# Kernel optimization log

Hardware: AMD Instinct MI355X
Metric: run time of the kernel (lower is better)

## Reference

```python
import jax, jax.numpy as jnp
import numpy as np

# Production-scale 3D conv: B=4, C=64->64, 32^3 volume, 3x3x3 kernel, stride 1, pad 1.
B, CIN, COUT = 4, 64, 64
KSIZE = (3, 3, 3)
STRIDE = (1, 1, 1)
PAD = 1
SPATIAL = (32, 32, 32)


def setup_inputs() -> dict:
    key = jax.random.key(0)
    k1, k2, k3 = jax.random.split(key, 3)
    x = jax.random.normal(k1, (B, CIN) + SPATIAL, dtype=jnp.float32)
    weight = jax.random.normal(k2, (COUT, CIN) + KSIZE, dtype=jnp.float32)
    bias = jax.random.normal(k3, (COUT,), dtype=jnp.float32)
    return {"x": x, "weight": weight, "bias": bias}


def reference(x, weight, bias):
    # The original materializes all sliding-window patches via nested unfold and
    # contracts with einsum('bci...,oci->bo...'). That is exactly a standard
    # cross-correlation (torch-style conv). We express the same math as a direct
    # convolution, avoiding the O(kernel_volume) patch blowup.
    out = jax.lax.conv_general_dilated(
        x,
        weight,
        window_strides=STRIDE,
        padding=[(PAD, PAD)] * 3,
        dimension_numbers=("NCDHW", "OIDHW", "NCDHW"),
    )
    return out + bias.reshape(1, -1, 1, 1, 1)
```

## Files before the change

kernel.cpp:

```cpp
#include <hip/hip_runtime.h>
#include <hip/hip_bf16.h>

#define WS_W_OFF    0
#define WS_ZERO_OFF 221184
#define WS_XT_OFF   262144

typedef __attribute__((ext_vector_type(8))) short s16x8;
typedef __attribute__((ext_vector_type(4))) float f32x4;

#define GLOBAL_AS __attribute__((address_space(1)))
#define LDS_AS    __attribute__((address_space(3)))

__device__ __forceinline__ unsigned short f2bf(float f) {
  unsigned u = __builtin_bit_cast(unsigned, f);
  u = u + 0x7fffu + ((u >> 16) & 1u);
  return (unsigned short)(u >> 16);
}

__global__ void prep_kernel(const float* __restrict__ x,
                            const float* __restrict__ w,
                            unsigned short* __restrict__ wsw,
                            float* __restrict__ zeros,
                            unsigned short* __restrict__ xt) {
  int blk = blockIdx.x;
  if (blk < 432) {
    int t = blk * 256 + threadIdx.x;
    int tap  = t % 27;
    int cin  = (t / 27) & 63;
    int cout = t / (27 * 64);
    int h   = cin >> 5;
    int q   = (cin >> 3) & 3;
    int j   = cin & 7;
    int nf  = cout >> 4;
    int lane = q * 16 + (cout & 15);
    int dst = (((tap * 2 + h) * 4 + nf) * 64 + lane) * 8 + j;
    wsw[dst] = f2bf(w[t]);
    if (t < 64) zeros[t] = 0.0f;
  } else {
    int t  = (blk - 432) * 256 + threadIdx.x;
    int s  = t & 32767;
    int c8 = (t >> 15) & 7;
    int b  = t >> 18;
    const float* src = x + (size_t)(b * 64 + c8 * 8) * 32768 + s;
    s16x8 v;
    #pragma unroll
    for (int k = 0; k < 8; ++k) v[k] = (short)f2bf(src[(size_t)k * 32768]);
    *(s16x8*)(xt + (size_t)(b * 32768 + s) * 64 + c8 * 8) = v;
  }
}

__global__ __launch_bounds__(128, 2) void conv_kernel(const float* __restrict__ bias,
                                                      float* __restrict__ out,
                                                      const char* __restrict__ ws) {
  __shared__ unsigned char halo[39 * 1024];

  const int tid  = threadIdx.x;
  const int lane = tid & 63;
  const int w    = tid >> 6;
  const int logical = (blockIdx.x & 7) * 128 + (blockIdx.x >> 3);
  const int yt = logical & 7, z = (logical >> 3) & 31, b = logical >> 8;
  const int y0 = yt * 4;

  const int r15 = lane & 15;
  const int hi4 = lane >> 4;

  const int sl_sub   = lane >> 2;
  const int sl_chunk = lane & 3;

  auto stage = [&](int h) {
    for (int g = w; g < 39; g += 2) {
      int pos = g * 16 + sl_sub;
      int hz = pos / 204; int rem = pos - hz * 204;
      int hy = rem / 34;  int hx = rem - hy * 34;
      int gz = z + hz - 1, gy = y0 + hy - 1, gx = hx - 1;
      bool inb = (pos < 612) & ((unsigned)gz < 32u) &
                 ((unsigned)gy < 32u) & ((unsigned)gx < 32u);
      int s = (gz * 32 + gy) * 32 + gx;
      int src = inb ? (WS_XT_OFF + (b * 32768 + s) * 128 + h * 64 + sl_chunk * 16)
                    : WS_ZERO_OFF;
      __builtin_amdgcn_global_load_lds(
          (const GLOBAL_AS void*)(ws + src),
          (LDS_AS void*)(&halo[g * 1024 + lane * 16]),
          16, 0, 0);
    }
  };

  const s16x8* __restrict__ wfr = (const s16x8*)(ws + WS_W_OFF);

  f32x4 zero4 = {0.f, 0.f, 0.f, 0.f};
  f32x4 acc[4][4];
  #pragma unroll
  for (int mf = 0; mf < 4; ++mf)
    #pragma unroll
    for (int nf = 0; nf < 4; ++nf) acc[mf][nf] = zero4;

  s16x8 B0[4], B1[4], A0[4], A1[4];

  auto loadB = [&](s16x8* dst, int h, int tap) {
    #pragma unroll
    for (int nf = 0; nf < 4; ++nf)
      dst[nf] = wfr[((tap * 2 + h) * 4 + nf) * 64 + lane];
  };

  auto loadA = [&](s16x8* a, int tap) {
    int kd = tap / 9; int r9 = tap - kd * 9;
    int kh = r9 / 3;  int kw = r9 - kh * 3;
    int prow = (kd * 6 + 2 * w + kh) * 34 + kw + r15;
    #pragma unroll
    for (int mf = 0; mf < 4; ++mf) {
      int pos = prow + (mf >> 1) * 34 + (mf & 1) * 16;
      a[mf] = *(const s16x8*)&halo[pos * 64 + hi4 * 16];
    }
  };

  auto compute = [&](const s16x8* a, const s16x8* B) {
    #pragma unroll
    for (int mf = 0; mf < 4; ++mf)
      #pragma unroll
      for (int nf = 0; nf < 4; ++nf)
        acc[mf][nf] = __builtin_amdgcn_mfma_f32_16x16x32_bf16(
            a[mf], B[nf], acc[mf][nf], 0, 0, 0);
  };

  #pragma unroll 1
  for (int h = 0; h < 2; ++h) {
    if (h) __syncthreads();
    stage(h);
    loadB(B0, h, 0);
    __syncthreads();
    loadA(A0, 0);
    for (int t = 0; t < 13; ++t) {
      loadB(B1, h, 2 * t + 1); loadA(A1, 2 * t + 1); compute(A0, B0);
      loadB(B0, h, 2 * t + 2); loadA(A0, 2 * t + 2); compute(A1, B1);
    }
    compute(A0, B0);
  }

  #pragma unroll
  for (int nf = 0; nf < 4; ++nf) {
    int cout = nf * 16 + r15;
    float bv = bias[cout];
    #pragma unroll
    for (int mf = 0; mf < 4; ++mf) {
      int y  = y0 + 2 * w + (mf >> 1);
      int x0 = (mf & 1) * 16 + 4 * hi4;
      float* orow = out + ((size_t)((b * 64 + cout) * 32 + z) * 32 + y) * 32;
      f32x4 v;
      #pragma unroll
      for (int r = 0; r < 4; ++r) v[r] = acc[mf][nf][r] + bv;
      *(f32x4*)&orow[x0] = v;
    }
  }
}

extern "C" void kernel_launch(void* const* d_in, const int* in_sizes, int n_in,
                              void* d_out, int out_size, void* d_ws, size_t ws_size,
                              hipStream_t stream) {
  const float* x    = (const float*)d_in[0];
  const float* wgt  = (const float*)d_in[1];
  const float* bias = (const float*)d_in[2];
  float* out = (float*)d_out;
  char* ws = (char*)d_ws;

  prep_kernel<<<4528, 256, 0, stream>>>(x, wgt,
                                        (unsigned short*)(ws + WS_W_OFF),
                                        (float*)(ws + WS_ZERO_OFF),
                                        (unsigned short*)(ws + WS_XT_OFF));
  conv_kernel<<<1024, 128, 0, stream>>>(bias, out, ws);
}
```

Baseline: 49.07 us.

## Tile two z-slices per block with four waves and triple-buffer tap loads

Each block now computes a 2×4×32 output tile (two z planes) with four waves instead of one z plane with two waves. The staged halo grows from 3 to 4 z-planes, so the halo load per output point drops, since neighbouring z planes share two input planes. The tap loop becomes a three-stage rotating register buffer for A and B fragments, with B preloaded before the barrier. The cost is more LDS per block (52 KB), which may limit occupancy, more registers for the extra buffers, and only 512 blocks, which reduces parallelism across CUs.

```diff
diff --git a/kernel.cpp b/kernel.cpp
--- a/kernel.cpp
+++ b/kernel.cpp
@@ -49,17 +49,19 @@
   }
 }
 
-__global__ __launch_bounds__(128, 2) void conv_kernel(const float* __restrict__ bias,
+__global__ __launch_bounds__(256, 2) void conv_kernel(const float* __restrict__ bias,
                                                       float* __restrict__ out,
                                                       const char* __restrict__ ws) {
-  __shared__ unsigned char halo[39 * 1024];
+  __shared__ unsigned char halo[52 * 1024];
 
   const int tid  = threadIdx.x;
   const int lane = tid & 63;
   const int w    = tid >> 6;
-  const int logical = (blockIdx.x & 7) * 128 + (blockIdx.x >> 3);
-  const int yt = logical & 7, z = (logical >> 3) & 31, b = logical >> 8;
-  const int y0 = yt * 4;
+  const int logical = (blockIdx.x & 7) * 64 + (blockIdx.x >> 3);
+  const int yt = logical & 7, zt = (logical >> 3) & 15, b = logical >> 7;
+  const int z0 = zt * 2, y0 = yt * 4;
+  const int zo  = w >> 1;
+  const int yo2 = (w & 1) * 2;
 
   const int r15 = lane & 15;
   const int hi4 = lane >> 4;
@@ -68,12 +70,12 @@
   const int sl_chunk = lane & 3;
 
   auto stage = [&](int h) {
-    for (int g = w; g < 39; g += 2) {
+    for (int g = w; g < 52; g += 4) {
       int pos = g * 16 + sl_sub;
       int hz = pos / 204; int rem = pos - hz * 204;
       int hy = rem / 34;  int hx = rem - hy * 34;
-      int gz = z + hz - 1, gy = y0 + hy - 1, gx = hx - 1;
-      bool inb = (pos < 612) & ((unsigned)gz < 32u) &
+      int gz = z0 + hz - 1, gy = y0 + hy - 1, gx = hx - 1;
+      bool inb = (pos < 816) & ((unsigned)gz < 32u) &
                  ((unsigned)gy < 32u) & ((unsigned)gx < 32u);
       int s = (gz * 32 + gy) * 32 + gx;
       int src = inb ? (WS_XT_OFF + (b * 32768 + s) * 128 + h * 64 + sl_chunk * 16)
@@ -94,7 +96,7 @@
     #pragma unroll
     for (int nf = 0; nf < 4; ++nf) acc[mf][nf] = zero4;
 
-  s16x8 B0[4], B1[4], A0[4], A1[4];
+  s16x8 B0[4], B1[4], B2[4], A0[4], A1[4], A2[4];
 
   auto loadB = [&](s16x8* dst, int h, int tap) {
     #pragma unroll
@@ -105,10 +107,10 @@
   auto loadA = [&](s16x8* a, int tap) {
     int kd = tap / 9; int r9 = tap - kd * 9;
     int kh = r9 / 3;  int kw = r9 - kh * 3;
-    int prow = (kd * 6 + 2 * w + kh) * 34 + kw + r15;
+    int base = ((zo + kd) * 6 + (yo2 + kh)) * 34 + kw + r15;
     #pragma unroll
     for (int mf = 0; mf < 4; ++mf) {
-      int pos = prow + (mf >> 1) * 34 + (mf & 1) * 16;
+      int pos = base + (mf >> 1) * 34 + (mf & 1) * 16;
       a[mf] = *(const s16x8*)&halo[pos * 64 + hi4 * 16];
     }
   };
@@ -122,27 +124,38 @@
             a[mf], B[nf], acc[mf][nf], 0, 0, 0);
   };
 
-  #pragma unroll 1
-  for (int h = 0; h < 2; ++h) {
-    if (h) __syncthreads();
-    stage(h);
-    loadB(B0, h, 0);
-    __syncthreads();
+  auto khalf = [&](int h) {
     loadA(A0, 0);
-    for (int t = 0; t < 13; ++t) {
-      loadB(B1, h, 2 * t + 1); loadA(A1, 2 * t + 1); compute(A0, B0);
-      loadB(B0, h, 2 * t + 2); loadA(A0, 2 * t + 2); compute(A1, B1);
+    #pragma unroll 1
+    for (int t = 0; t < 8; ++t) {
+      loadB(B2, h, 3 * t + 2); loadA(A1, 3 * t + 1); compute(A0, B0);
+      loadB(B0, h, 3 * t + 3); loadA(A2, 3 * t + 2); compute(A1, B1);
+      loadB(B1, h, 3 * t + 4); loadA(A0, 3 * t + 3); compute(A2, B2);
     }
-    compute(A0, B0);
-  }
+    loadB(B2, h, 26); loadA(A1, 25); compute(A0, B0);
+    loadA(A2, 26);    compute(A1, B1);
+    compute(A2, B2);
+  };
 
+  stage(0);
+  loadB(B0, 0, 0); loadB(B1, 0, 1);
+  __syncthreads();
+  khalf(0);
+
+  loadB(B0, 1, 0); loadB(B1, 1, 1);
+  __syncthreads();
+  stage(1);
+  __syncthreads();
+  khalf(1);
+
+  const int z = z0 + zo;
   #pragma unroll
   for (int nf = 0; nf < 4; ++nf) {
     int cout = nf * 16 + r15;
     float bv = bias[cout];
     #pragma unroll
     for (int mf = 0; mf < 4; ++mf) {
-      int y  = y0 + 2 * w + (mf >> 1);
+      int y  = y0 + yo2 + (mf >> 1);
       int x0 = (mf & 1) * 16 + 4 * hi4;
       float* orow = out + ((size_t)((b * 64 + cout) * 32 + z) * 32 + y) * 32;
       f32x4 v;
@@ -166,5 +179,5 @@
                                         (unsigned short*)(ws + WS_W_OFF),
                                         (float*)(ws + WS_ZERO_OFF),
                                         (unsigned short*)(ws + WS_XT_OFF));
-  conv_kernel<<<1024, 128, 0, stream>>>(bias, out, ws);
+  conv_kernel<<<512, 256, 0, stream>>>(bias, out, ws);
 }
```

Result: faster. 46.20 us (-5.8%).

## Use 1024-thread blocks covering 4x4 z-y tiles with split-K reduction in LDS

Applied to the files above, without the earlier changes.

Restructures the conv kernel so each block of 16 waves covers a 4(z)x4(y) output tile and stages the full 64-channel halo once, with an XOR swizzle to avoid LDS bank conflicts. The two input-channel halves are split across wave pairs and their partial sums are reduced through LDS before the output write. This removes the second staging pass and the redundant halo loads across z. In exchange, only 256 blocks are launched, the LDS footprint is large at about 153KB, and the explicit A/B prefetch double-buffering is replaced by a fully unrolled tap loop.

```diff
diff --git a/kernel.cpp b/kernel.cpp
--- a/kernel.cpp
+++ b/kernel.cpp
@@ -49,41 +49,45 @@
   }
 }
 
-__global__ __launch_bounds__(128, 2) void conv_kernel(const float* __restrict__ bias,
-                                                      float* __restrict__ out,
-                                                      const char* __restrict__ ws) {
-  __shared__ unsigned char halo[39 * 1024];
+__global__ __launch_bounds__(1024, 4) void conv_kernel(const float* __restrict__ bias,
+                                                       float* __restrict__ out,
+                                                       const char* __restrict__ ws) {
+  __shared__ __align__(16) unsigned char halo[1224 * 128];
 
   const int tid  = threadIdx.x;
   const int lane = tid & 63;
   const int w    = tid >> 6;
-  const int logical = (blockIdx.x & 7) * 128 + (blockIdx.x >> 3);
-  const int yt = logical & 7, z = (logical >> 3) & 31, b = logical >> 8;
-  const int y0 = yt * 4;
+  const int t_   = w >> 1;
+  const int h    = w & 1;
+  const int zi   = t_ >> 1, yi = t_ & 1;
+  const int logical = (blockIdx.x & 7) * 32 + (blockIdx.x >> 3);
+  const int yq = logical & 7, zq = (logical >> 3) & 7, b = logical >> 6;
+  const int z0 = zq * 4, y0 = yq * 4;
 
   const int r15 = lane & 15;
   const int hi4 = lane >> 4;
 
-  const int sl_sub   = lane >> 2;
-  const int sl_chunk = lane & 3;
-
-  auto stage = [&](int h) {
-    for (int g = w; g < 39; g += 2) {
-      int pos = g * 16 + sl_sub;
-      int hz = pos / 204; int rem = pos - hz * 204;
-      int hy = rem / 34;  int hx = rem - hy * 34;
-      int gz = z + hz - 1, gy = y0 + hy - 1, gx = hx - 1;
-      bool inb = (pos < 612) & ((unsigned)gz < 32u) &
-                 ((unsigned)gy < 32u) & ((unsigned)gx < 32u);
-      int s = (gz * 32 + gy) * 32 + gx;
-      int src = inb ? (WS_XT_OFF + (b * 32768 + s) * 128 + h * 64 + sl_chunk * 16)
-                    : WS_ZERO_OFF;
-      __builtin_amdgcn_global_load_lds(
-          (const GLOBAL_AS void*)(ws + src),
-          (LDS_AS void*)(&halo[g * 1024 + lane * 16]),
-          16, 0, 0);
+  {
+    const int csrc = ((tid & 7) ^ ((tid >> 3) & 7)) * 16;
+    #pragma unroll 1
+    for (int r = 0; r < 10; ++r) {
+      int pos = r * 128 + (tid >> 3);
+      if (pos < 1224) {
+        int hz = pos / 204; int rem = pos - hz * 204;
+        int hy = rem / 34;  int hx = rem - hy * 34;
+        int gz = z0 + hz - 1, gy = y0 + hy - 1, gx = hx - 1;
+        bool inb = ((unsigned)gz < 32u) & ((unsigned)gy < 32u) &
+                   ((unsigned)gx < 32u);
+        int s = (gz * 32 + gy) * 32 + gx;
+        int src = inb ? (WS_XT_OFF + (b * 32768 + s) * 128 + csrc)
+                      : WS_ZERO_OFF;
+        __builtin_amdgcn_global_load_lds(
+            (const GLOBAL_AS void*)(ws + src),
+            (LDS_AS void*)(&halo[r * 16384 + tid * 16]),
+            16, 0, 0);
+      }
     }
-  };
+  }
 
   const s16x8* __restrict__ wfr = (const s16x8*)(ws + WS_W_OFF);
 
@@ -94,60 +98,61 @@
     #pragma unroll
     for (int nf = 0; nf < 4; ++nf) acc[mf][nf] = zero4;
 
-  s16x8 B0[4], B1[4], A0[4], A1[4];
+  const int pbase = (zi * 6 + yi * 2) * 34 + r15;
+  const int chunk = h * 4 + hi4;
 
-  auto loadB = [&](s16x8* dst, int h, int tap) {
+  __syncthreads();
+
+  #pragma unroll
+  for (int tap = 0; tap < 27; ++tap) {
+    const int kd = tap / 9, r9 = tap % 9;
+    const int kh = r9 / 3, kw = r9 % 3;
+    s16x8 Bf[4], Af[4];
     #pragma unroll
     for (int nf = 0; nf < 4; ++nf)
-      dst[nf] = wfr[((tap * 2 + h) * 4 + nf) * 64 + lane];
-  };
-
-  auto loadA = [&](s16x8* a, int tap) {
-    int kd = tap / 9; int r9 = tap - kd * 9;
-    int kh = r9 / 3;  int kw = r9 - kh * 3;
-    int prow = (kd * 6 + 2 * w + kh) * 34 + kw + r15;
+      Bf[nf] = wfr[((tap * 2 + h) * 4 + nf) * 64 + lane];
     #pragma unroll
     for (int mf = 0; mf < 4; ++mf) {
-      int pos = prow + (mf >> 1) * 34 + (mf & 1) * 16;
-      a[mf] = *(const s16x8*)&halo[pos * 64 + hi4 * 16];
+      int p = pbase + (kd * 6 + (mf >> 1) + kh) * 34 + kw + (mf & 1) * 16;
+      Af[mf] = *(const s16x8*)&halo[p * 128 + ((chunk ^ (p & 7)) << 4)];
     }
-  };
-
-  auto compute = [&](const s16x8* a, const s16x8* B) {
     #pragma unroll
     for (int mf = 0; mf < 4; ++mf)
       #pragma unroll
       for (int nf = 0; nf < 4; ++nf)
         acc[mf][nf] = __builtin_amdgcn_mfma_f32_16x16x32_bf16(
-            a[mf], B[nf], acc[mf][nf], 0, 0, 0);
-  };
-
-  #pragma unroll 1
-  for (int h = 0; h < 2; ++h) {
-    if (h) __syncthreads();
-    stage(h);
-    loadB(B0, h, 0);
-    __syncthreads();
-    loadA(A0, 0);
-    for (int t = 0; t < 13; ++t) {
-      loadB(B1, h, 2 * t + 1); loadA(A1, 2 * t + 1); compute(A0, B0);
-      loadB(B0, h, 2 * t + 2); loadA(A0, 2 * t + 2); compute(A1, B1);
-    }
-    compute(A0, B0);
+            Af[mf], Bf[nf], acc[mf][nf], 0, 0, 0);
   }
 
+  __syncthreads();
+  {
+    unsigned char* red = halo;
+    const int wrOff = t_ * 16384 + (1 - h) * 8192;
+    #pragma unroll
+    for (int mfr = 0; mfr < 2; ++mfr)
+      #pragma unroll
+      for (int nf = 0; nf < 4; ++nf)
+        *(f32x4*)&red[wrOff + (mfr * 4 + nf) * 1024 + lane * 16] =
+            acc[(1 - h) * 2 + mfr][nf];
+  }
+  __syncthreads();
+
+  const int z = z0 + zi;
+  const int y = y0 + yi * 2 + h;
+  const int rdOff = t_ * 16384 + h * 8192;
   #pragma unroll
   for (int nf = 0; nf < 4; ++nf) {
     int cout = nf * 16 + r15;
     float bv = bias[cout];
+    float* orow = out + ((size_t)((b * 64 + cout) * 32 + z) * 32 + y) * 32;
     #pragma unroll
-    for (int mf = 0; mf < 4; ++mf) {
-      int y  = y0 + 2 * w + (mf >> 1);
-      int x0 = (mf & 1) * 16 + 4 * hi4;
-      float* orow = out + ((size_t)((b * 64 + cout) * 32 + z) * 32 + y) * 32;
+    for (int mfr = 0; mfr < 2; ++mfr) {
+      f32x4 part = *(const f32x4*)&halo[rdOff + (mfr * 4 + nf) * 1024 + lane * 16];
+      int x0 = mfr * 16 + hi4 * 4;
       f32x4 v;
       #pragma unroll
-      for (int r = 0; r < 4; ++r) v[r] = acc[mf][nf][r] + bv;
+      for (int r = 0; r < 4; ++r)
+        v[r] = acc[h * 2 + mfr][nf][r] + part[r] + bv;
       *(f32x4*)&orow[x0] = v;
     }
   }
@@ -166,5 +171,5 @@
                                         (unsigned short*)(ws + WS_W_OFF),
                                         (float*)(ws + WS_ZERO_OFF),
                                         (unsigned short*)(ws + WS_XT_OFF));
-  conv_kernel<<<1024, 128, 0, stream>>>(bias, out, ws);
+  conv_kernel<<<256, 1024, 0, stream>>>(bias, out, ws);
 }
```

Result: slower. 69.94 us (+42.5%).
